# Optimization experiments

Measured on AMD Instinct MI355X. Metric: run time of the kernel, lower is better.

The kernel has to match this reference:

```python
import jax, jax.numpy as jnp
import numpy as np

B, S, D_IN, D_OUT, H = 2, 2048, 1024, 1024, 16
HD = D_OUT // H  # 64


def setup_inputs() -> dict:
    key = jax.random.key(0)
    ks = jax.random.split(key, 6)
    s = 0.02
    return {
        "x": jax.random.normal(ks[0], (B, S, D_IN), dtype=jnp.float32),
        "W_q": jax.random.normal(ks[1], (D_IN, D_OUT), dtype=jnp.float32) * s,
        "W_k": jax.random.normal(ks[2], (D_IN, D_OUT), dtype=jnp.float32) * s,
        "W_v": jax.random.normal(ks[3], (D_IN, D_OUT), dtype=jnp.float32) * s,
        "W_o": jax.random.normal(ks[4], (D_OUT, D_OUT), dtype=jnp.float32) * s,
        "b_o": jax.random.normal(ks[5], (D_OUT,), dtype=jnp.float32) * s,
    }


def reference(x, W_q, W_k, W_v, W_o, b_o):
    b, n, _ = x.shape
    # project and split heads: [b, h, n, hd]
    q = (x @ W_q).reshape(b, n, H, HD).transpose(0, 2, 1, 3)
    k = (x @ W_k).reshape(b, n, H, HD).transpose(0, 2, 1, 3)
    v = (x @ W_v).reshape(b, n, H, HD).transpose(0, 2, 1, 3)
    scores = jnp.einsum("bhqd,bhkd->bhqk", q, k) / jnp.sqrt(jnp.float32(HD))
    causal = jnp.tril(jnp.ones((n, n), dtype=bool))
    scores = jnp.where(causal, scores, -jnp.inf)
    attn = jax.nn.softmax(scores, axis=-1)  # dropout p=0.0 -> identity
    ctx = jnp.einsum("bhqk,bhkd->bhqd", attn, v)
    ctx = ctx.transpose(0, 2, 1, 3).reshape(b, n, D_OUT)
    return ctx @ W_o + b_o
```

## Files before the change

kernel.cpp:

```cpp
#include <hip/hip_runtime.h>

#define B_    2
#define S_    2048
#define DIN   1024
#define DOUT  1024
#define H_    16
#define HD_   64
#define M_    (B_ * S_)

typedef __bf16 bf16x8 __attribute__((ext_vector_type(8)));
typedef float  f32x4  __attribute__((ext_vector_type(4)));

__device__ __forceinline__ f32x4 MFMA(bf16x8 a, bf16x8 b, f32x4 c) {
    return __builtin_amdgcn_mfma_f32_16x16x32_bf16(a, b, c, 0, 0, 0);
}

__device__ __forceinline__ unsigned short f2b(float f) {
    union { float f; unsigned int u; } v; v.f = f;
    unsigned int u = v.u;
    return (unsigned short)((u + 0x7fffu + ((u >> 16) & 1u)) >> 16);
}

__device__ __forceinline__ unsigned pack2(float a, float b) {
    union { __bf16 h[2]; unsigned u; } cv;
    cv.h[0] = (__bf16)a; cv.h[1] = (__bf16)b;
    return cv.u;
}

#define GLDS(gp, lp) __builtin_amdgcn_global_load_lds( \
    (const __attribute__((address_space(1))) void*)(gp), \
    (__attribute__((address_space(3))) void*)(lp), 16, 0, 0)

#define QSCALE 0.1803368801111204f

__global__ __launch_bounds__(256) void k_cvt_all(const float* __restrict__ x,
                                                 const float* __restrict__ Wq,
                                                 const float* __restrict__ Wk,
                                                 const float* __restrict__ Wv,
                                                 const float* __restrict__ Wo,
                                                 unsigned short* __restrict__ xb,
                                                 unsigned short* __restrict__ WqkvT,
                                                 unsigned short* __restrict__ WoT) {
    __shared__ __align__(16) float tile[64][68];
    int bid = blockIdx.x;
    int tid = threadIdx.x;
    if (bid < 1024) {
#pragma unroll
        for (int j = 0; j < 4; j++) {
            int i = bid * 4096 + j * 1024 + tid * 4;
            float4 v = *reinterpret_cast<const float4*>(x + i);
            ushort4 o;
            o.x = f2b(v.x); o.y = f2b(v.y); o.z = f2b(v.z); o.w = f2b(v.w);
            *reinterpret_cast<ushort4*>(xb + i) = o;
        }
        return;
    }
    int wb = bid - 1024;
    int w = wb >> 8;
    int t = wb & 255;
    const float* src = (w == 0) ? Wq : (w == 1) ? Wk : (w == 2) ? Wv : Wo;
    unsigned short* dst = (w < 3) ? WqkvT + (size_t)w * 1024 * DIN : WoT;
    int k0 = (t >> 4) * 64, n0 = (t & 15) * 64;
#pragma unroll
    for (int j = 0; j < 4; j++) {
        int idx = j * 256 + tid;
        int r = idx >> 4, c4g = idx & 15;
        int sg = c4g ^ ((r >> 3) & 7);
        *reinterpret_cast<float4*>(&tile[r][sg * 4]) =
            *reinterpret_cast<const float4*>(&src[(size_t)(k0 + r) * DOUT + n0 + c4g * 4]);
    }
    __syncthreads();
#pragma unroll
    for (int j = 0; j < 2; j++) {
        int idx = j * 256 + tid;
        int n = idx >> 3, gk = (idx & 7) * 8;
        int g = n >> 2, e = n & 3;
        unsigned short o[8];
#pragma unroll
        for (int u = 0; u < 8; u++) {
            int k = gk + u;
            o[u] = f2b(tile[k][((g ^ ((k >> 3) & 7)) << 2) + e]);
        }
        *reinterpret_cast<int4*>(&dst[(size_t)(n0 + n) * DIN + k0 + gk]) =
            *reinterpret_cast<int4*>(o);
    }
}

template <int OUT_MODE, int BM>
__global__ __launch_bounds__(256) void k_gemm(const unsigned short* __restrict__ A,
                                              const unsigned short* __restrict__ Bt,
                                              unsigned short* __restrict__ Cq,
                                              unsigned short* __restrict__ Ck,
                                              unsigned short* __restrict__ Cvt,
                                              float* __restrict__ Cf,
                                              const float* __restrict__ bias,
                                              int M, int N, int K, int bxg) {
    constexpr int MI  = BM / 32;
    constexpr int ASZ = BM * 32;
    constexpr int BSZ = 128 * 32;
    constexpr int ACH = BM / 64;
    constexpr int STG = 3 * (ASZ + BSZ);
    constexpr int SMEM_N = (OUT_MODE == 0 && STG < 17408) ? 17408 : STG;
    __shared__ __align__(16) unsigned short smem[SMEM_N];

    int bid = blockIdx.x;
    int xcd = bid & 7;
    int r = bid >> 3;
    int byg = (M / BM) >> 2;
    int by = (xcd >> 1) * byg + r / bxg;
    int bx = (xcd & 1) * bxg + r % bxg;
    int m0 = by * BM, n0 = bx * 128;

    int tid = threadIdx.x;
    int wid = tid >> 6, lane = tid & 63;
    int wm = wid >> 1, wn = wid & 1;
    int lr = lane & 15, lg = lane >> 4;

    f32x4 acc[MI][4] = {};

    int srow = lane >> 2;
    int scol = ((lane & 3) ^ (srow & 3)) * 8;
    int runit = (lg ^ (lr & 3)) * 8;

#define STAGE_G(buf, k0)                                                       \
    {                                                                          \
        unsigned short* Ad = smem + (buf) * ASZ;                               \
        unsigned short* Bd = smem + 3 * ASZ + (buf) * BSZ;                     \
        _Pragma("unroll")                                                      \
        for (int c = 0; c < ACH; c++) {                                        \
            int chunk = wid * ACH + c;                                         \
            int row = chunk * 16 + srow;                                       \
            GLDS(A + (size_t)(m0 + row) * K + (k0) + scol,                     \
                 (char*)Ad + chunk * 1024);                                    \
        }                                                                      \
        _Pragma("unroll")                                                      \
        for (int c = 0; c < 2; c++) {                                          \
            int chunk = wid * 2 + c;                                           \
            int row = chunk * 16 + srow;                                       \
            GLDS(Bt + (size_t)(n0 + row) * K + (k0) + scol,                    \
                 (char*)Bd + chunk * 1024);                                    \
        }                                                                      \
    }

    int nkt = K >> 5;
    STAGE_G(0, 0)

    int cur = 0;
    for (int kt = 0; kt < nkt; kt++) {
        if (kt + 1 < nkt) {
            int nb = cur + 1; if (nb >= 3) nb -= 3;
            STAGE_G(nb, (kt + 1) * 32)
            if constexpr (BM == 128) { asm volatile("s_waitcnt vmcnt(4)" ::: "memory"); }
            else                     { asm volatile("s_waitcnt vmcnt(3)" ::: "memory"); }
        } else {
            asm volatile("s_waitcnt vmcnt(0)" ::: "memory");
        }
        __builtin_amdgcn_s_barrier();

        const unsigned short* Asr = smem + cur * ASZ;
        const unsigned short* Bsr = smem + 3 * ASZ + cur * BSZ;
        bf16x8 af[MI], bf[4];
#pragma unroll
        for (int mi = 0; mi < MI; mi++)
            af[mi] = *reinterpret_cast<const bf16x8*>(
                &Asr[(wm * (BM / 2) + mi * 16 + lr) * 32 + runit]);
#pragma unroll
        for (int ni = 0; ni < 4; ni++)
            bf[ni] = *reinterpret_cast<const bf16x8*>(
                &Bsr[(wn * 64 + ni * 16 + lr) * 32 + runit]);
#pragma unroll
        for (int mi = 0; mi < MI; mi++)
#pragma unroll
            for (int ni = 0; ni < 4; ni++)
                acc[mi][ni] = MFMA(af[mi], bf[ni], acc[mi][ni]);

        cur = cur + 1; if (cur >= 3) cur -= 3;
    }

    if (OUT_MODE == 2) {
        for (int mi = 0; mi < MI; mi++)
            for (int ni = 0; ni < 4; ni++)
                for (int i = 0; i < 4; i++) {
                    int row = m0 + wm * (BM / 2) + mi * 16 + lg * 4 + i;
                    int col = n0 + wn * 64 + ni * 16 + lr;
                    Cf[(size_t)row * N + col] = acc[mi][ni][i] + bias[col];
                }
    } else if (n0 < 2048) {
        unsigned short* Cd = (n0 < 1024) ? Cq : Ck;
        int cb = (n0 < 1024) ? 0 : 1024;
        float sc = (n0 < 1024) ? QSCALE : 1.0f;
        for (int mi = 0; mi < MI; mi++)
            for (int ni = 0; ni < 4; ni++)
                for (int i = 0; i < 4; i++) {
                    int row = m0 + wm * (BM / 2) + mi * 16 + lg * 4 + i;
                    int col = n0 + wn * 64 + ni * 16 + lr;
                    Cd[(size_t)row * 1024 + (col - cb)] = f2b(acc[mi][ni][i] * sc);
                }
    } else {
        __syncthreads();
        unsigned short* Lt = smem;
        for (int mi = 0; mi < MI; mi++)
            for (int ni = 0; ni < 4; ni++) {
                int cl = wn * 64 + ni * 16 + lr;
                int rl0 = wm * (BM / 2) + mi * 16 + lg * 4;
                uint2 wd;
                wd.x = pack2(acc[mi][ni][0], acc[mi][ni][1]);
                wd.y = pack2(acc[mi][ni][2], acc[mi][ni][3]);
                *reinterpret_cast<uint2*>(&Lt[cl * 136 + rl0]) = wd;
            }
        __syncthreads();
        int b = m0 >> 11, ms = m0 & (S_ - 1);
        int bh64 = (b * H_ + ((n0 - 2048) >> 6)) * 64;
#pragma unroll
        for (int it = 0; it < 4; it++) {
            int cl = it * 32 + (tid >> 3);
            int ss = (tid & 7) * 16;
            int4 v0 = *reinterpret_cast<int4*>(&Lt[cl * 136 + ss]);
            int4 v1 = *reinterpret_cast<int4*>(&Lt[cl * 136 + ss + 8]);
            unsigned short* dp = Cvt + (size_t)(bh64 + cl) * S_ + ms + ss;
            *reinterpret_cast<int4*>(dp) = v0;
            *reinterpret_cast<int4*>(dp + 8) = v1;
        }
    }
#undef STAGE_G
}

__global__ __launch_bounds__(512, 4) void k_attn(const unsigned short* __restrict__ Q,
                                                 const unsigned short* __restrict__ Kg,
                                                 const unsigned short* __restrict__ Vt,
                                                 unsigned short* __restrict__ ctx) {
    int bid = blockIdx.x;
    int xcd = bid & 7;
    int k   = bid >> 3;
    int p   = k >> 2;
    int bh  = xcd * 4 + (k & 3);
    int b = bh >> 4, h = bh & 15;
    int tid = threadIdx.x, wid = tid >> 6, lane = tid & 63;
    int lr = lane & 15, lg = lane >> 4;
    int qtB = 31 - p;
    int qt = (wid < 4) ? qtB : p;
    int q0 = qt * 64 + (wid & 3) * 16;

    __shared__ __align__(16) unsigned short Ks[4][64 * 64];
    __shared__ __align__(16) unsigned short Vs[4][64 * 64];
    __shared__ __align__(16) unsigned p_lds32[8][16 * 32];
    unsigned* pl32 = p_lds32[wid];

    const unsigned short* Qp = Q  + (size_t)b * S_ * DOUT + (size_t)h * HD_;
    const unsigned short* Kp = Kg + (size_t)b * S_ * DOUT + (size_t)h * HD_;
    const unsigned short* Vp = Vt + (size_t)(b * H_ + h) * HD_ * S_;

    bf16x8 qf0 = *reinterpret_cast<const bf16x8*>(&Qp[(size_t)(q0 + lr) * DOUT + lg * 8]);
    bf16x8 qf1 = *reinterpret_cast<const bf16x8*>(&Qp[(size_t)(q0 + lr) * DOUT + 32 + lg * 8]);
    asm volatile("" : "+v"(qf0), "+v"(qf1));

    int srow = lane >> 3;
    int scol = ((lane & 7) ^ srow) * 8;

#define STAGE_KV(buf, t)                                                           \
    {                                                                              \
        int kv0_ = (t) * 64;                                                       \
        int krow = wid * 8 + srow;                                                 \
        GLDS(Kp + (size_t)(kv0_ + krow) * DOUT + scol,                             \
             (char*)&Ks[buf][0] + wid * 1024);                                     \
        GLDS(Vp + (size_t)krow * S_ + kv0_ + scol,                                 \
             (char*)&Vs[buf][0] + wid * 1024);                                     \
    }

    int ntile = qtB + 1;
    STAGE_KV(0, 0)
    STAGE_KV(1, 1)

    f32x4 o[4] = {};
    float l = 0.f;
    int rxor = (lr & 7) << 4;
    int qg = q0 + lr;

    int cur = 0;
    for (int t = 0; t < ntile; t++) {
        int ahead = ntile - 1 - t;
        if (ahead >= 2) {
            STAGE_KV((cur + 2) & 3, t + 2)
            asm volatile("s_waitcnt vmcnt(4)" ::: "memory");
        } else if (ahead == 1) {
            asm volatile("s_waitcnt vmcnt(2)" ::: "memory");
        } else {
            asm volatile("s_waitcnt vmcnt(0)" ::: "memory");
        }
        __builtin_amdgcn_s_barrier();

        if (t <= qt) {
            const unsigned short* Kt = Ks[cur];
            const unsigned short* Vl = Vs[cur];
            int kv0 = t * 64;

            f32x4 s[4] = {};
            __builtin_amdgcn_s_setprio(1);
#pragma unroll
            for (int nf = 0; nf < 4; nf++)
#pragma unroll
                for (int kk = 0; kk < 2; kk++) {
                    bf16x8 kf = *reinterpret_cast<const bf16x8*>(
                        &Kt[(nf * 16 + lr) * 64 + (((kk * 64 + lg * 16) ^ rxor) >> 1)]);
                    s[nf] = MFMA(kf, kk ? qf1 : qf0, s[nf]);
                }
            __builtin_amdgcn_s_setprio(0);

            if (t == qt) {
#pragma unroll
                for (int nf = 0; nf < 4; nf++)
#pragma unroll
                    for (int i = 0; i < 4; i++)
                        if (kv0 + nf * 16 + lg * 4 + i > qg) s[nf][i] = -2000.0f;
            }

            f32x4 acc = {};
#pragma unroll
            for (int nf = 0; nf < 4; nf++) {
                f32x4 pv;
#pragma unroll
                for (int i = 0; i < 4; i++) pv[i] = exp2f(s[nf][i]);
                acc += pv;
                int unit = (nf * 2 + (lg >> 1)) ^ (lr & 7);
                uint2 wd; wd.x = pack2(pv[0], pv[1]); wd.y = pack2(pv[2], pv[3]);
                *reinterpret_cast<uint2*>(&pl32[lr * 32 + unit * 4 + (lg & 1) * 2]) = wd;
            }
            l += (acc[0] + acc[1]) + (acc[2] + acc[3]);

            bf16x8 pf[2];
#pragma unroll
            for (int kvb = 0; kvb < 2; kvb++)
                pf[kvb] = *reinterpret_cast<const bf16x8*>(
                    &pl32[lr * 32 + (((kvb * 4 + lg) ^ (lr & 7)) * 4)]);

            __builtin_amdgcn_s_setprio(1);
#pragma unroll
            for (int nd = 0; nd < 4; nd++)
#pragma unroll
                for (int kk = 0; kk < 2; kk++) {
                    bf16x8 vf = *reinterpret_cast<const bf16x8*>(
                        &Vl[(nd * 16 + lr) * 64 + (((kk * 64 + lg * 16) ^ rxor) >> 1)]);
                    o[nd] = MFMA(pf[kk], vf, o[nd]);
                }
            __builtin_amdgcn_s_setprio(0);
        }

        cur = (cur + 1) & 3;
    }

    l += __shfl_xor(l, 16, 64);
    l += __shfl_xor(l, 32, 64);

#pragma unroll
    for (int i = 0; i < 4; i++) {
        float li = __shfl(l, lg * 4 + i, 16);
        float r = __builtin_amdgcn_rcpf(li);
#pragma unroll
        for (int nd = 0; nd < 4; nd++)
            ((__bf16*)ctx)[((size_t)b * S_ + q0 + lg * 4 + i) * DOUT + h * HD_ + nd * 16 + lr] =
                (__bf16)(o[nd][i] * r);
    }
#undef STAGE_KV
}

extern "C" void kernel_launch(void* const* d_in, const int* in_sizes, int n_in,
                              void* d_out, int out_size, void* d_ws, size_t ws_size,
                              hipStream_t stream) {
    const float* x  = (const float*)d_in[0];
    const float* Wq = (const float*)d_in[1];
    const float* Wk = (const float*)d_in[2];
    const float* Wv = (const float*)d_in[3];
    const float* Wo = (const float*)d_in[4];
    const float* bo = (const float*)d_in[5];
    float* out = (float*)d_out;
    char* ws = (char*)d_ws;
    const size_t MB = 1u << 20;

    unsigned short* xb    = (unsigned short*)(ws);
    unsigned short* ctx   = (unsigned short*)(ws);
    unsigned short* WqkvT = (unsigned short*)(ws + 8 * MB);
    unsigned short* WoT   = (unsigned short*)(ws + 14 * MB);
    unsigned short* Qb    = (unsigned short*)(ws + 16 * MB);
    unsigned short* Kb    = (unsigned short*)(ws + 24 * MB);
    unsigned short* Vtb   = (unsigned short*)(ws + 32 * MB);

    (void)in_sizes; (void)n_in; (void)out_size; (void)ws_size;

    k_cvt_all<<<2048, 256, 0, stream>>>(x, Wq, Wk, Wv, Wo, xb, WqkvT, WoT);

    k_gemm<0, 128><<<768, 256, 0, stream>>>(xb, WqkvT, Qb, Kb, Vtb, nullptr, nullptr,
                                            M_, 3072, DIN, 12);

    k_attn<<<512, 512, 0, stream>>>(Qb, Kb, Vtb, ctx);

    k_gemm<2, 64><<<512, 256, 0, stream>>>(ctx, WoT, nullptr, nullptr, nullptr,
                                           out, bo, M_, DOUT, DOUT, 4);
}
```

Before: 100.4 us.

## Software-pipeline next tile's QK^T with current tile's softmax and PV

Restructures the causal attention loop so the QK^T MFMAs for tile t+1 are issued before the exp/pack/PV work for tile t. The score accumulators are double-buffered (s_cur/s_next), and a prologue computes the first tile's scores. To make tile t+1 resident one iteration earlier, the wait after prefetching tile t+2 tightens from vmcnt(4) to vmcnt(2), which shortens the effective prefetch distance. It also adds 16 live fp32 registers per lane under a 512x4 launch bound, which risks spills or lower occupancy.

```diff
diff --git a/kernel.cpp b/kernel.cpp
--- a/kernel.cpp
+++ b/kernel.cpp
@@ -231,9 +231,9 @@
                                                  unsigned short* __restrict__ ctx) {
     int bid = blockIdx.x;
     int xcd = bid & 7;
-    int k   = bid >> 3;
-    int p   = k >> 2;
-    int bh  = xcd * 4 + (k & 3);
+    int kb  = bid >> 3;
+    int p   = kb >> 2;
+    int bh  = xcd * 4 + (kb & 3);
     int b = bh >> 4, h = bh & 15;
     int tid = threadIdx.x, wid = tid >> 6, lane = tid & 63;
     int lr = lane & 15, lg = lane >> 4;
@@ -267,6 +267,30 @@
              (char*)&Vs[buf][0] + wid * 1024);                                     \
     }
 
+#define QKT(sarr, Kt, tt)                                                          \
+    {                                                                              \
+        _Pragma("unroll")                                                          \
+        for (int nf = 0; nf < 4; nf++) sarr[nf] = (f32x4){};                       \
+        __builtin_amdgcn_s_setprio(1);                                             \
+        _Pragma("unroll")                                                          \
+        for (int nf = 0; nf < 4; nf++)                                             \
+            _Pragma("unroll")                                                      \
+            for (int kk = 0; kk < 2; kk++) {                                       \
+                bf16x8 kf = *reinterpret_cast<const bf16x8*>(                      \
+                    &(Kt)[(nf * 16 + lr) * 64 + (((kk * 64 + lg * 16) ^ rxor) >> 1)]); \
+                sarr[nf] = MFMA(kf, kk ? qf1 : qf0, sarr[nf]);                     \
+            }                                                                      \
+        __builtin_amdgcn_s_setprio(0);                                             \
+        if ((tt) == qt) {                                                          \
+            int kv0_ = (tt) * 64;                                                  \
+            _Pragma("unroll")                                                      \
+            for (int nf = 0; nf < 4; nf++)                                         \
+                _Pragma("unroll")                                                  \
+                for (int i = 0; i < 4; i++)                                        \
+                    if (kv0_ + nf * 16 + lg * 4 + i > qg) sarr[nf][i] = -2000.0f;  \
+        }                                                                          \
+    }
+
     int ntile = qtB + 1;
     STAGE_KV(0, 0)
     STAGE_KV(1, 1)
@@ -276,50 +300,30 @@
     int rxor = (lr & 7) << 4;
     int qg = q0 + lr;
 
-    int cur = 0;
+    f32x4 s_cur[4], s_next[4];
+
+    asm volatile("s_waitcnt vmcnt(2)" ::: "memory");
+    __builtin_amdgcn_s_barrier();
+    QKT(s_cur, Ks[0], 0)
+
     for (int t = 0; t < ntile; t++) {
-        int ahead = ntile - 1 - t;
-        if (ahead >= 2) {
-            STAGE_KV((cur + 2) & 3, t + 2)
-            asm volatile("s_waitcnt vmcnt(4)" ::: "memory");
-        } else if (ahead == 1) {
+        if (t + 2 < ntile) {
+            STAGE_KV((t + 2) & 3, t + 2)
             asm volatile("s_waitcnt vmcnt(2)" ::: "memory");
         } else {
             asm volatile("s_waitcnt vmcnt(0)" ::: "memory");
         }
         __builtin_amdgcn_s_barrier();
 
+        if (t + 1 <= qt) QKT(s_next, Ks[(t + 1) & 3], t + 1)
+
         if (t <= qt) {
-            const unsigned short* Kt = Ks[cur];
-            const unsigned short* Vl = Vs[cur];
-            int kv0 = t * 64;
-
-            f32x4 s[4] = {};
-            __builtin_amdgcn_s_setprio(1);
-#pragma unroll
-            for (int nf = 0; nf < 4; nf++)
-#pragma unroll
-                for (int kk = 0; kk < 2; kk++) {
-                    bf16x8 kf = *reinterpret_cast<const bf16x8*>(
-                        &Kt[(nf * 16 + lr) * 64 + (((kk * 64 + lg * 16) ^ rxor) >> 1)]);
-                    s[nf] = MFMA(kf, kk ? qf1 : qf0, s[nf]);
-                }
-            __builtin_amdgcn_s_setprio(0);
-
-            if (t == qt) {
-#pragma unroll
-                for (int nf = 0; nf < 4; nf++)
-#pragma unroll
-                    for (int i = 0; i < 4; i++)
-                        if (kv0 + nf * 16 + lg * 4 + i > qg) s[nf][i] = -2000.0f;
-            }
-
             f32x4 acc = {};
 #pragma unroll
             for (int nf = 0; nf < 4; nf++) {
                 f32x4 pv;
 #pragma unroll
-                for (int i = 0; i < 4; i++) pv[i] = exp2f(s[nf][i]);
+                for (int i = 0; i < 4; i++) pv[i] = exp2f(s_cur[nf][i]);
                 acc += pv;
                 int unit = (nf * 2 + (lg >> 1)) ^ (lr & 7);
                 uint2 wd; wd.x = pack2(pv[0], pv[1]); wd.y = pack2(pv[2], pv[3]);
@@ -333,6 +337,7 @@
                 pf[kvb] = *reinterpret_cast<const bf16x8*>(
                     &pl32[lr * 32 + (((kvb * 4 + lg) ^ (lr & 7)) * 4)]);
 
+            const unsigned short* Vl = Vs[t & 3];
             __builtin_amdgcn_s_setprio(1);
 #pragma unroll
             for (int nd = 0; nd < 4; nd++)
@@ -345,7 +350,8 @@
             __builtin_amdgcn_s_setprio(0);
         }
 
-        cur = (cur + 1) & 3;
+#pragma unroll
+        for (int j = 0; j < 4; j++) s_cur[j] = s_next[j];
     }
 
     l += __shfl_xor(l, 16, 64);
@@ -361,6 +367,7 @@
                 (__bf16)(o[nd][i] * r);
     }
 #undef STAGE_KV
+#undef QKT
 }
 
 extern "C" void kernel_launch(void* const* d_in, const int* in_sizes, int n_in,
```

After: 101.1 us. About the same (+0.8%).
